# Optimization experiments

Hardware: AMD Instinct MI355X
Metric: run time of the kernel (lower is better)

Reference implementation:

```python
import jax, jax.numpy as jnp
import numpy as np

H = 128          # hidden_size
IN = 93          # input_size
NL = 4           # num_layers
B, T = 256, 512  # batch, seq_len


def setup_inputs() -> dict:
    key = jax.random.key(0)
    ks = jax.random.split(key, 8)
    s = 1.0 / np.sqrt(H)  # pytorch LSTM init range scale
    x = jax.random.normal(ks[0], (B, T, IN), jnp.float32)
    W_ih0 = jax.random.normal(ks[1], (4 * H, IN), jnp.float32) * s   # layer 0 input weights
    W_ih_rest = jax.random.normal(ks[2], (NL - 1, 4 * H, H), jnp.float32) * s  # layers 1..3
    W_hh = jax.random.normal(ks[3], (NL, 4 * H, H), jnp.float32) * s
    b_ih = jax.random.normal(ks[4], (NL, 4 * H), jnp.float32) * s
    b_hh = jax.random.normal(ks[5], (NL, 4 * H), jnp.float32) * s
    W_fc = jax.random.normal(ks[6], (1, H), jnp.float32) * s
    b_fc = jax.random.normal(ks[7], (1,), jnp.float32) * s
    return {"x": x, "W_ih0": W_ih0, "W_ih_rest": W_ih_rest, "W_hh": W_hh,
            "b_ih": b_ih, "b_hh": b_hh, "W_fc": W_fc, "b_fc": b_fc}


def _lstm_layer(x_tm, W_ih, W_hh_l, bi, bh):
    # x_tm: [T, B, in]; precompute input-side gates as one big GEMM
    gates_x = jnp.einsum('tbi,gi->tbg', x_tm, W_ih) + bi + bh  # [T,B,4H]

    def step(carry, gx):
        h, c = carry
        g = gx + h @ W_hh_l.T                      # [B,4H]
        i, f, gg, o = jnp.split(g, 4, axis=-1)     # pytorch gate order: i,f,g,o
        i = jax.nn.sigmoid(i)
        f = jax.nn.sigmoid(f)
        gg = jnp.tanh(gg)
        o = jax.nn.sigmoid(o)
        c = f * c + i * gg
        h = o * jnp.tanh(c)
        return (h, c), h

    b = x_tm.shape[1]
    h0 = jnp.zeros((b, H), x_tm.dtype)
    (_, _), hs = jax.lax.scan(step, (h0, h0), gates_x)
    return hs  # [T,B,H]


def reference(x, W_ih0, W_ih_rest, W_hh, b_ih, b_hh, W_fc, b_fc):
    # Eval-mode forward (dropout inactive), matching model.eval() semantics.
    h = jnp.transpose(x, (1, 0, 2))  # time-major [T,B,IN]
    h = _lstm_layer(h, W_ih0, W_hh[0], b_ih[0], b_hh[0])
    for l in range(1, NL):
        h = _lstm_layer(h, W_ih_rest[l - 1], W_hh[l], b_ih[l], b_hh[l])
    out = jax.nn.sigmoid(jnp.einsum('tbh,oh->tbo', h, W_fc) + b_fc)  # [T,B,1]
    return jnp.transpose(out, (1, 0, 2))  # [B,T,1]
```

## Files before the change

kernel.cpp:

```cpp
#include <hip/hip_runtime.h>
#include <hip/hip_bf16.h>

#define H_    128
#define IN_   93
#define NL_   4
#define B_    256
#define T_    512
#define G_    512
#define W_    32
#define LOG2E 1.44269504088896f

typedef __attribute__((ext_vector_type(8))) short bf16x8;
typedef __attribute__((ext_vector_type(4))) float f32x4;
typedef unsigned long long u64;

#define RING_SLOT (H_ * B_)
#define RING_L    ((size_t)W_ * RING_SLOT)

__device__ __forceinline__ ushort bf16_rn(float f) {
    uint x = __float_as_uint(f);
    uint r = (x + 0x7FFFu + ((x >> 16) & 1u)) >> 16;
    return (ushort)r;
}
__device__ __forceinline__ float exp2_fast(float x) { return __builtin_amdgcn_exp2f(x); }
__device__ __forceinline__ float rcp_fast(float x)  { return __builtin_amdgcn_rcpf(x); }
__device__ __forceinline__ float sig_y(float y)  { return rcp_fast(1.0f + exp2_fast(-y)); }
__device__ __forceinline__ float tanh_y(float y) { return __builtin_fmaf(2.0f, rcp_fast(1.0f + exp2_fast(-y)), -1.0f); }

__device__ __forceinline__ int spin_ge(int* p, int target) {
    int v = __hip_atomic_load(p, __ATOMIC_ACQUIRE, __HIP_MEMORY_SCOPE_AGENT);
    while (v < target) {
        __builtin_amdgcn_s_sleep(8);
        v = __hip_atomic_load(p, __ATOMIC_ACQUIRE, __HIP_MEMORY_SCOPE_AGENT);
    }
    return v;
}

__global__ void prep_x(const float* __restrict__ x, ushort* __restrict__ xb) {
    int idx = blockIdx.x * 256 + threadIdx.x;
    int t = idx / (B_ * 96);
    int rem = idx % (B_ * 96);
    int b = rem / 96;
    int k = rem % 96;
    float v = 0.0f;
    if (k < IN_) v = x[((size_t)b * T_ + t) * IN_ + k];
    xb[idx] = bf16_rn(v);
}

__global__ void prep_w(const float* __restrict__ Wih0,
                       const float* __restrict__ Wihr,
                       const float* __restrict__ Whh,
                       ushort* __restrict__ Wc) {
    int idx = blockIdx.x * 256 + threadIdx.x;
    int l = idx / (G_ * 256);
    int rem = idx % (G_ * 256);
    int g = rem / 256;
    int k = rem % 256;
    int kx = (l == 0) ? 96 : 128;
    float v = 0.0f;
    if (k < kx) {
        if (l == 0) { if (k < IN_) v = Wih0[g * IN_ + k]; }
        else        { v = Wihr[(((size_t)(l - 1)) * G_ + g) * H_ + k]; }
    } else if (k < kx + H_) {
        v = Whh[(((size_t)l) * G_ + g) * H_ + (k - kx)];
    }
    float scale = (g >= 256 && g < 384) ? (2.0f * LOG2E) : LOG2E;
    Wc[idx] = bf16_rn(v * scale);
}

__global__ void prep_bias(const float* __restrict__ bih,
                          const float* __restrict__ bhh,
                          float* __restrict__ bc) {
    int idx = blockIdx.x * 256 + threadIdx.x;
    int g = idx & 511;
    float scale = (g >= 256 && g < 384) ? (2.0f * LOG2E) : LOG2E;
    bc[idx] = (bih[idx] + bhh[idx]) * scale;
}

__global__ void zero_prog(int* __restrict__ prog) {
    int i = threadIdx.x;
    for (int k = i; k < NL_ * 16 * 16; k += 256) prog[k] = 0;
}

__global__ __launch_bounds__(512, 2)
void recur_all(const ushort* __restrict__ xb,
               const ushort* __restrict__ Wc,
               const float* __restrict__ biasc,
               ushort* __restrict__ ring,
               ushort* __restrict__ h3,
               int* __restrict__ prog) {
    __shared__ ushort comb[2][16][272];

    const int bid = blockIdx.x;
    const int l = bid >> 4;
    const int g = bid & 15;
    const int kx = (l == 0) ? 96 : 128;

    const int tid = threadIdx.x;
    const int w   = tid >> 6;
    const int ln  = tid & 63;
    const int q   = ln >> 4;
    const int lo  = ln & 15;
    const int u   = (w << 4) | lo;
    const int b0  = g << 4;

    const ushort* Wl = Wc + (size_t)l * G_ * 256;
    const float*  bl = biasc + l * G_;
    int* prog_self = prog + (l * 16 + g) * 16;
    int* prog_up   = prog + ((l - 1) * 16 + g) * 16;
    int* prog_down = prog + ((l + 1) * 16 + g) * 16;

    for (int i = tid; i < 2 * 16 * 272; i += 512) ((ushort*)comb)[i] = 0;

    bf16x8 bw[4][8];
#pragma unroll
    for (int tu = 0; tu < 4; ++tu)
#pragma unroll
        for (int s = 0; s < 8; ++s) {
            const ushort* pp = Wl + ((size_t)((tu << 7) + u) << 8) + (s << 5) + (q << 3);
            bw[tu][s] = *(const bf16x8*)pp;
        }

    const float bv0 = bl[u];
    const float bv1 = bl[128 + u];
    const float bv2 = bl[256 + u];
    const float bv3 = bl[384 + u];

    f32x4 cc = {0.0f, 0.0f, 0.0f, 0.0f};

    const int srow = tid >> 5;
    const int seg  = tid & 31;
    const bool act = (seg < 24);
    const int uu = tid >> 2;
    const int r4 = (tid & 3) << 2;

    uint2 xr = {0u, 0u};
    u64 hx = 0;
    int avail = 0;

    if (l == 0) {
        if (act) xr = *(const uint2*)(xb + (size_t)(b0 + srow) * 96 + (seg << 2));
    } else {
        avail = spin_ge(prog_up, 1);
        const u64* sp = (const u64*)(ring + (size_t)(l - 1) * RING_L + (size_t)uu * B_ + (b0 + r4));
        hx = __hip_atomic_load((u64*)sp, __ATOMIC_RELAXED, __HIP_MEMORY_SCOPE_AGENT);
    }

    __syncthreads();

    for (int t = 0; t < T_; ++t) {
        const int p = t & 1;

        if (l == 0) {
            if (act) *(uint2*)&comb[p][srow][seg << 2] = xr;
        } else {
#pragma unroll
            for (int j = 0; j < 4; ++j)
                comb[p][r4 + j][uu] = (ushort)(hx >> (16 * j));
        }

        __syncthreads();

        if (tid == 0 && t > 0)
            __hip_atomic_store(prog_self, t, __ATOMIC_RELAXED, __HIP_MEMORY_SCOPE_AGENT);
        if (l < 3 && t >= W_ && (t & 15) == 0)
            (void)spin_ge(prog_down, t - 16);

        if (t < T_ - 1) {
            if (l == 0) {
                if (act) xr = *(const uint2*)(xb + (size_t)((t + 1) * B_ + b0 + srow) * 96 + (seg << 2));
            } else {
                if (avail < t + 2) {
                    int tgt = t + 8; if (tgt > T_) tgt = T_;
                    avail = spin_ge(prog_up, tgt);
                }
                const u64* sp = (const u64*)(ring + (size_t)(l - 1) * RING_L +
                                             (size_t)((t + 1) & (W_ - 1)) * RING_SLOT +
                                             (size_t)uu * B_ + (b0 + r4));
                hx = __hip_atomic_load((u64*)sp, __ATOMIC_RELAXED, __HIP_MEMORY_SCOPE_AGENT);
            }
        }

        f32x4 a0 = {bv0, bv0, bv0, bv0};
        f32x4 a1 = {bv1, bv1, bv1, bv1};
        f32x4 a2 = {bv2, bv2, bv2, bv2};
        f32x4 a3 = {bv3, bv3, bv3, bv3};
#pragma unroll
        for (int s = 0; s < 8; ++s) {
            bf16x8 av = *(const bf16x8*)&comb[p][lo][(s << 5) + (q << 3)];
            a0 = __builtin_amdgcn_mfma_f32_16x16x32_bf16(av, bw[0][s], a0, 0, 0, 0);
            a1 = __builtin_amdgcn_mfma_f32_16x16x32_bf16(av, bw[1][s], a1, 0, 0, 0);
            a2 = __builtin_amdgcn_mfma_f32_16x16x32_bf16(av, bw[2][s], a2, 0, 0, 0);
            a3 = __builtin_amdgcn_mfma_f32_16x16x32_bf16(av, bw[3][s], a3, 0, 0, 0);
        }

        u64 hv = 0;
#pragma unroll
        for (int r = 0; r < 4; ++r) {
            float i_ = sig_y(a0[r]);
            float f_ = sig_y(a1[r]);
            float g_ = tanh_y(a2[r]);
            float o_ = sig_y(a3[r]);
            float cn = __builtin_fmaf(f_, cc[r], i_ * g_);
            cc[r] = cn;
            float th = tanh_y(2.88539008177793f * cn);
            float h_ = o_ * th;
            ushort hb = bf16_rn(h_);
            comb[p ^ 1][(q << 2) + r][kx + u] = hb;
            hv |= (u64)hb << (16 * r);
        }
        if (l < 3) {
            u64* dst = (u64*)(ring + (size_t)l * RING_L +
                              (size_t)(t & (W_ - 1)) * RING_SLOT +
                              (size_t)u * B_ + (b0 + (q << 2)));
            __hip_atomic_store(dst, hv, __ATOMIC_RELAXED, __HIP_MEMORY_SCOPE_AGENT);
        } else {
            *(u64*)(h3 + (size_t)t * RING_SLOT + (size_t)u * B_ + (b0 + (q << 2))) = hv;
        }
    }

    __syncthreads();
    if (tid == 0)
        __hip_atomic_store(prog_self, T_, __ATOMIC_RELAXED, __HIP_MEMORY_SCOPE_AGENT);
}

__global__ void fc_kernel(const ushort* __restrict__ h3,
                          const float* __restrict__ wfc,
                          const float* __restrict__ bfc,
                          float* __restrict__ out) {
    int t = blockIdx.x;
    int b = threadIdx.x;
    const ushort* hp = h3 + (size_t)t * RING_SLOT + b;
    float acc = 0.0f;
#pragma unroll 8
    for (int u = 0; u < H_; ++u) {
        float hv = __uint_as_float(((uint)hp[(size_t)u * B_]) << 16);
        acc = __builtin_fmaf(hv, wfc[u], acc);
    }
    float z = acc + bfc[0];
    out[(size_t)b * T_ + t] = rcp_fast(1.0f + exp2_fast(-z * LOG2E));
}

extern "C" void kernel_launch(void* const* d_in, const int* in_sizes, int n_in,
                              void* d_out, int out_size, void* d_ws, size_t ws_size,
                              hipStream_t stream) {
    const float* x    = (const float*)d_in[0];
    const float* Wih0 = (const float*)d_in[1];
    const float* Wihr = (const float*)d_in[2];
    const float* Whh  = (const float*)d_in[3];
    const float* bih  = (const float*)d_in[4];
    const float* bhh  = (const float*)d_in[5];
    const float* Wfc  = (const float*)d_in[6];
    const float* bfc  = (const float*)d_in[7];
    float* out = (float*)d_out;

    char* ws = (char*)d_ws;
    const size_t xb_bytes   = (size_t)T_ * B_ * 96 * 2;
    const size_t wc_bytes   = (size_t)NL_ * G_ * 256 * 2;
    const size_t bias_bytes = (size_t)NL_ * G_ * 4;
    const size_t prog_bytes = (size_t)NL_ * 16 * 16 * 4;
    const size_t ring_bytes = (size_t)3 * RING_L * 2;

    ushort* xb    = (ushort*)ws;
    ushort* Wc    = (ushort*)(ws + xb_bytes);
    float*  biasc = (float*)(ws + xb_bytes + wc_bytes);
    int*    prog  = (int*)(ws + xb_bytes + wc_bytes + bias_bytes);
    ushort* ring  = (ushort*)(ws + xb_bytes + wc_bytes + bias_bytes + prog_bytes);
    ushort* h3    = (ushort*)(ws + xb_bytes + wc_bytes + bias_bytes + prog_bytes + ring_bytes);

    prep_x<<<(T_ * B_ * 96) / 256, 256, 0, stream>>>(x, xb);
    prep_w<<<(NL_ * G_ * 256) / 256, 256, 0, stream>>>(Wih0, Wihr, Whh, Wc);
    prep_bias<<<(NL_ * G_) / 256, 256, 0, stream>>>(bih, bhh, biasc);
    zero_prog<<<1, 256, 0, stream>>>(prog);

    recur_all<<<NL_ * 16, 512, 0, stream>>>(xb, Wc, biasc, ring, h3, prog);

    fc_kernel<<<T_, B_, 0, stream>>>(h3, Wfc, bfc, out);
}
```

Baseline: 987.5 us.

## Switch ring buffer to batch-major layout, defer h stores, fuse gate reciprocals

The inter-layer ring buffer and h3 move from unit-major to batch-major layout. Each step's hidden state is now stored from LDS in the next iteration with one contiguous 64-bit write per thread instead of scattered per-unit writes, and consumer threads load 64-bit rows straight into the LDS combine buffer. The gate activations are rewritten to share reciprocals: i*g and o*tanh(c) each use one rcp of a product of denominators, with clamped exponents. Other changes: shorter spin sleep, progress signalling shifted by one step with adjusted thresholds, and an FC kernel that reads vectorized rows. The lagged publication adds a step of pipeline latency between layers.

```diff
diff --git a/kernel.cpp b/kernel.cpp
--- a/kernel.cpp
+++ b/kernel.cpp
@@ -14,7 +14,7 @@
 typedef __attribute__((ext_vector_type(4))) float f32x4;
 typedef unsigned long long u64;
 
-#define RING_SLOT (H_ * B_)
+#define RING_SLOT (B_ * H_)
 #define RING_L    ((size_t)W_ * RING_SLOT)
 
 __device__ __forceinline__ ushort bf16_rn(float f) {
@@ -24,13 +24,11 @@
 }
 __device__ __forceinline__ float exp2_fast(float x) { return __builtin_amdgcn_exp2f(x); }
 __device__ __forceinline__ float rcp_fast(float x)  { return __builtin_amdgcn_rcpf(x); }
-__device__ __forceinline__ float sig_y(float y)  { return rcp_fast(1.0f + exp2_fast(-y)); }
-__device__ __forceinline__ float tanh_y(float y) { return __builtin_fmaf(2.0f, rcp_fast(1.0f + exp2_fast(-y)), -1.0f); }
 
 __device__ __forceinline__ int spin_ge(int* p, int target) {
     int v = __hip_atomic_load(p, __ATOMIC_ACQUIRE, __HIP_MEMORY_SCOPE_AGENT);
     while (v < target) {
-        __builtin_amdgcn_s_sleep(8);
+        __builtin_amdgcn_s_sleep(2);
         v = __hip_atomic_load(p, __ATOMIC_ACQUIRE, __HIP_MEMORY_SCOPE_AGENT);
     }
     return v;
@@ -110,6 +108,9 @@
     int* prog_up   = prog + ((l - 1) * 16 + g) * 16;
     int* prog_down = prog + ((l + 1) * 16 + g) * 16;
 
+    ushort* ring_self = ring + (size_t)l * RING_L;
+    const ushort* ring_up = ring + (size_t)(l - 1) * RING_L;
+
     for (int i = tid; i < 2 * 16 * 272; i += 512) ((ushort*)comb)[i] = 0;
 
     bf16x8 bw[4][8];
@@ -128,22 +129,21 @@
 
     f32x4 cc = {0.0f, 0.0f, 0.0f, 0.0f};
 
-    const int srow = tid >> 5;
+    const int crow = tid >> 5;
+    const int cu4  = (tid & 31) << 2;
     const int seg  = tid & 31;
     const bool act = (seg < 24);
-    const int uu = tid >> 2;
-    const int r4 = (tid & 3) << 2;
 
     uint2 xr = {0u, 0u};
     u64 hx = 0;
     int avail = 0;
 
     if (l == 0) {
-        if (act) xr = *(const uint2*)(xb + (size_t)(b0 + srow) * 96 + (seg << 2));
+        if (act) xr = *(const uint2*)(xb + (size_t)(b0 + crow) * 96 + (seg << 2));
     } else {
-        avail = spin_ge(prog_up, 1);
-        const u64* sp = (const u64*)(ring + (size_t)(l - 1) * RING_L + (size_t)uu * B_ + (b0 + r4));
-        hx = __hip_atomic_load((u64*)sp, __ATOMIC_RELAXED, __HIP_MEMORY_SCOPE_AGENT);
+        avail = spin_ge(prog_up, (9 < T_) ? 9 : T_);
+        hx = __hip_atomic_load((u64*)(ring_up + (size_t)(b0 + crow) * H_ + cu4),
+                               __ATOMIC_RELAXED, __HIP_MEMORY_SCOPE_AGENT);
     }
 
     __syncthreads();
@@ -152,32 +152,41 @@
         const int p = t & 1;
 
         if (l == 0) {
-            if (act) *(uint2*)&comb[p][srow][seg << 2] = xr;
+            if (act) *(uint2*)&comb[p][crow][seg << 2] = xr;
         } else {
-#pragma unroll
-            for (int j = 0; j < 4; ++j)
-                comb[p][r4 + j][uu] = (ushort)(hx >> (16 * j));
+            *(u64*)&comb[p][crow][cu4] = hx;
         }
 
         __syncthreads();
 
-        if (tid == 0 && t > 0)
-            __hip_atomic_store(prog_self, t, __ATOMIC_RELAXED, __HIP_MEMORY_SCOPE_AGENT);
-        if (l < 3 && t >= W_ && (t & 15) == 0)
-            (void)spin_ge(prog_down, t - 16);
+        if (tid == 0 && t >= 1)
+            __hip_atomic_store(prog_self, t - 1, __ATOMIC_RELAXED, __HIP_MEMORY_SCOPE_AGENT);
+
+        if (t >= 1) {
+            u64 hold = *(const u64*)&comb[p][crow][kx + cu4];
+            if (l < 3) {
+                u64* dst = (u64*)(ring_self + (size_t)((t - 1) & (W_ - 1)) * RING_SLOT +
+                                  (size_t)(b0 + crow) * H_ + cu4);
+                __hip_atomic_store(dst, hold, __ATOMIC_RELAXED, __HIP_MEMORY_SCOPE_AGENT);
+            } else {
+                *(u64*)(h3 + (size_t)(t - 1) * RING_SLOT + (size_t)(b0 + crow) * H_ + cu4) = hold;
+            }
+        }
+
+        if (l < 3 && t >= 32 && (t & 15) == 0)
+            (void)spin_ge(prog_down, t - 17);
 
         if (t < T_ - 1) {
             if (l == 0) {
-                if (act) xr = *(const uint2*)(xb + (size_t)((t + 1) * B_ + b0 + srow) * 96 + (seg << 2));
+                if (act) xr = *(const uint2*)(xb + (size_t)((t + 1) * B_ + b0 + crow) * 96 + (seg << 2));
             } else {
                 if (avail < t + 2) {
-                    int tgt = t + 8; if (tgt > T_) tgt = T_;
+                    int tgt = t + 9; if (tgt > T_) tgt = T_;
                     avail = spin_ge(prog_up, tgt);
                 }
-                const u64* sp = (const u64*)(ring + (size_t)(l - 1) * RING_L +
-                                             (size_t)((t + 1) & (W_ - 1)) * RING_SLOT +
-                                             (size_t)uu * B_ + (b0 + r4));
-                hx = __hip_atomic_load((u64*)sp, __ATOMIC_RELAXED, __HIP_MEMORY_SCOPE_AGENT);
+                hx = __hip_atomic_load((u64*)(ring_up + (size_t)((t + 1) & (W_ - 1)) * RING_SLOT +
+                                              (size_t)(b0 + crow) * H_ + cu4),
+                                       __ATOMIC_RELAXED, __HIP_MEMORY_SCOPE_AGENT);
             }
         }
 
@@ -194,31 +203,34 @@
             a3 = __builtin_amdgcn_mfma_f32_16x16x32_bf16(av, bw[3][s], a3, 0, 0, 0);
         }
 
-        u64 hv = 0;
 #pragma unroll
         for (int r = 0; r < 4; ++r) {
-            float i_ = sig_y(a0[r]);
-            float f_ = sig_y(a1[r]);
-            float g_ = tanh_y(a2[r]);
-            float o_ = sig_y(a3[r]);
-            float cn = __builtin_fmaf(f_, cc[r], i_ * g_);
+            float ei = exp2_fast(fminf(-a0[r], 60.0f));
+            float ef = exp2_fast(-a1[r]);
+            float eg = exp2_fast(fminf(-a2[r], 60.0f));
+            float eo = exp2_fast(fminf(-a3[r], 60.0f));
+            float rf  = rcp_fast(1.0f + ef);
+            float rig = rcp_fast((1.0f + ei) * (1.0f + eg));
+            float cn  = __builtin_fmaf(cc[r], rf, (1.0f - eg) * rig);
             cc[r] = cn;
-            float th = tanh_y(2.88539008177793f * cn);
-            float h_ = o_ * th;
-            ushort hb = bf16_rn(h_);
-            comb[p ^ 1][(q << 2) + r][kx + u] = hb;
-            hv |= (u64)hb << (16 * r);
-        }
+            float ec  = exp2_fast(fminf(-2.88539008177793f * cn, 60.0f));
+            float roc = rcp_fast((1.0f + eo) * (1.0f + ec));
+            float h_  = (1.0f - ec) * roc;
+            comb[p ^ 1][(q << 2) + r][kx + u] = bf16_rn(h_);
+        }
+    }
+
+    __syncthreads();
+    {
+        u64 hold = *(const u64*)&comb[T_ & 1][crow][kx + cu4];
         if (l < 3) {
-            u64* dst = (u64*)(ring + (size_t)l * RING_L +
-                              (size_t)(t & (W_ - 1)) * RING_SLOT +
-                              (size_t)u * B_ + (b0 + (q << 2)));
-            __hip_atomic_store(dst, hv, __ATOMIC_RELAXED, __HIP_MEMORY_SCOPE_AGENT);
+            u64* dst = (u64*)(ring_self + (size_t)((T_ - 1) & (W_ - 1)) * RING_SLOT +
+                              (size_t)(b0 + crow) * H_ + cu4);
+            __hip_atomic_store(dst, hold, __ATOMIC_RELAXED, __HIP_MEMORY_SCOPE_AGENT);
         } else {
-            *(u64*)(h3 + (size_t)t * RING_SLOT + (size_t)u * B_ + (b0 + (q << 2))) = hv;
-        }
-    }
-
+            *(u64*)(h3 + (size_t)(T_ - 1) * RING_SLOT + (size_t)(b0 + crow) * H_ + cu4) = hold;
+        }
+    }
     __syncthreads();
     if (tid == 0)
         __hip_atomic_store(prog_self, T_, __ATOMIC_RELAXED, __HIP_MEMORY_SCOPE_AGENT);
@@ -230,12 +242,19 @@
                           float* __restrict__ out) {
     int t = blockIdx.x;
     int b = threadIdx.x;
-    const ushort* hp = h3 + (size_t)t * RING_SLOT + b;
+    const uint4* hp = (const uint4*)(h3 + ((size_t)t * B_ + b) * H_);
     float acc = 0.0f;
-#pragma unroll 8
-    for (int u = 0; u < H_; ++u) {
-        float hv = __uint_as_float(((uint)hp[(size_t)u * B_]) << 16);
-        acc = __builtin_fmaf(hv, wfc[u], acc);
+#pragma unroll
+    for (int kk = 0; kk < 16; ++kk) {
+        uint4 pv = hp[kk];
+        const uint vv[4] = {pv.x, pv.y, pv.z, pv.w};
+#pragma unroll
+        for (int j = 0; j < 4; ++j) {
+            float f0 = __uint_as_float(vv[j] << 16);
+            float f1 = __uint_as_float(vv[j] & 0xFFFF0000u);
+            acc = __builtin_fmaf(f0, wfc[kk * 8 + j * 2 + 0], acc);
+            acc = __builtin_fmaf(f1, wfc[kk * 8 + j * 2 + 1], acc);
+        }
     }
     float z = acc + bfc[0];
     out[(size_t)b * T_ + t] = rcp_fast(1.0f + exp2_fast(-z * LOG2E));
```

After: 976.4 us. Within noise of the previous version (-1.1%).
